# Optimization experiments

Measured on AMD Instinct MI355X. Metric: run time of the kernel, lower is better.

## Reference

```python
import jax, jax.numpy as jnp
import numpy as np

NS = 8          # neighborhood_size
PAD = NS // 2   # pad_size
BW = 0.5        # band_width
EPS_NORM = 1e-12  # F.normalize eps
EPS = 1e-5


def setup_inputs() -> dict:
    key = jax.random.key(0)
    k1, k2, k3, k4, k5 = jax.random.split(key, 5)
    N, C, H, W, D = 2, 48, 64, 64, 64
    S = 10  # num_samples
    x = jax.random.normal(k1, (N, C, H, W, D), dtype=jnp.float32)
    y = jax.random.normal(k2, (N, C, H, W, D), dtype=jnp.float32)
    # torch.randint(pad, H-pad) -> indices in [4, 60)
    h_indices = jax.random.randint(k3, (S,), PAD, H - PAD)
    w_indices = jax.random.randint(k4, (S,), PAD, W - PAD)
    d_indices = jax.random.randint(k5, (S,), PAD, D - PAD)
    return {"x": x, "y": y, "h_indices": h_indices,
            "w_indices": w_indices, "d_indices": d_indices}


def _contextual_loss_3d(x, y, h_idx, w_idx, d_idx):
    N, C = x.shape[0], x.shape[1]

    def slice_neigh(a, hi, wi, di):
        # 8x8x8 cube around (hi, wi, di) -> (N, C, NS, NS, NS)
        return jax.lax.dynamic_slice(
            a, (0, 0, hi - PAD, wi - PAD, di - PAD), (N, C, NS, NS, NS))

    def per_sample(hi, wi, di):
        xn = slice_neigh(x, hi, wi, di).reshape(N, C, -1)  # (N, C, M), M=512
        yn = slice_neigh(y, hi, wi, di).reshape(N, C, -1)
        y_mu = yn.mean(axis=(0, 2), keepdims=True)          # (1, C, 1)
        xc = xn - y_mu
        yc = yn - y_mu
        # F.normalize(p=2, dim=1): divide by max(||.||, eps)
        xc = xc / jnp.maximum(jnp.linalg.norm(xc, axis=1, keepdims=True), EPS_NORM)
        yc = yc / jnp.maximum(jnp.linalg.norm(yc, axis=1, keepdims=True), EPS_NORM)
        dist = 1.0 - jnp.einsum('ncm,ncp->nmp', xc, yc)     # (N, M, M)
        dist_min = dist.min(axis=2, keepdims=True)
        dist_tilde = dist / (dist_min + EPS)
        cx = jax.nn.softmax((1.0 - dist_tilde) / BW, axis=2)
        cx = cx.max(axis=1).mean(axis=1)                    # (N,)
        return jnp.mean(-jnp.log(cx + EPS))

    losses = jax.vmap(per_sample)(h_idx, w_idx, d_idx)      # (S,)
    return losses.mean()


def reference(x, y, h_indices, w_indices, d_indices):
    return _contextual_loss_3d(x, y, h_indices, w_indices, d_indices)
```

## Files before the change

kernel.cpp:

```cpp
#include <hip/hip_runtime.h>
#include <hip/hip_bf16.h>
#include <math.h>

#define S_    10
#define C_    48
#define HWD   64
#define M_    512
#define PADK  4
#define PAIRS 20

#define OFF_GY  0
#define OFF_GX  491520
#define OFF_CM  983040
#define OFF_MU  (OFF_CM + PAIRS * M_)
#define OFF_CNT (OFF_MU + 480)
#define OFF_ALL (OFF_CNT + 20)
#define OFF_PL  (OFF_ALL + 1)
#define OFF_YK  993824
#define OFF_XK  (OFF_YK + 327680)

typedef __attribute__((ext_vector_type(8))) short bf16x8;
typedef __attribute__((ext_vector_type(4))) float f32x4;

__device__ __forceinline__ int gidx(int n, int c, int h, int w, int d) {
  return (((n * C_ + c) * HWD + h) * HWD + w) * HWD + d;
}

__device__ __forceinline__ unsigned short f2bf(float f) {
  unsigned u = __float_as_uint(f);
  u += 0x7FFFu + ((u >> 16) & 1u);
  return (unsigned short)(u >> 16);
}

__device__ __forceinline__ int fidx(int m, int c) {
  return ((m >> 4) << 10) + ((c >> 5) << 9) + (((c >> 3) & 3) << 7) +
         ((m & 15) << 3) + (c & 7);
}

__global__ void k_gather(const float* __restrict__ x, const float* __restrict__ y,
                         const int* __restrict__ hi, const int* __restrict__ wi,
                         const int* __restrict__ di, float* __restrict__ ws) {
  int b = blockIdx.x, t = threadIdx.x;
  int lane = t & 63, wv = t >> 6;
  __shared__ float red[4];
  if (b < 40) ws[OFF_CM + b * 256 + t] = 0.f;
  if (b == 40 && t < 41) ws[OFF_CNT + t] = 0.f;
  int which = b >= 480;
  int r = which ? b - 480 : b;
  int s = r / C_, c = r % C_;
  const float* src = which ? x : y;
  int h0 = hi[s] - PADK, w0 = wi[s] - PADK, d0 = di[s] - PADK;
  float* dst = ws + (which ? OFF_GX : OFF_GY) + (s * 96 + 2 * c) * 512;
  float sum = 0.f;
#pragma unroll
  for (int j = 0; j < 4; ++j) {
    int i = t + 256 * j;
    int n = i >> 9, m = i & 511;
    float v = src[gidx(n, c, h0 + (m >> 6), w0 + ((m >> 3) & 7), d0 + (m & 7))];
    dst[n * 512 + m] = v;
    sum += v;
  }
  if (!which) {
#pragma unroll
    for (int off = 32; off; off >>= 1) sum += __shfl_xor(sum, off);
    if (lane == 0) red[wv] = sum;
    __syncthreads();
    if (t == 0)
      ws[OFF_MU + s * C_ + c] =
          (red[0] + red[1] + red[2] + red[3]) * (1.0f / 1024.0f);
  }
}

__global__ void k_nc(float* __restrict__ ws) {
  int g = blockIdx.x * 256 + threadIdx.x;
  int col = g >> 2;
  int q = threadIdx.x & 3;
  int which = col >= 10240;
  int cix = which ? col - 10240 : col;
  int pair = cix >> 9, m = cix & 511;
  int s = pair >> 1, n = pair & 1;
  const float* base = ws + (which ? OFF_GX : OFF_GY) + (s * 96 + n) * 512 + m;
  const float* mus = ws + OFF_MU + s * C_;
  int c0 = q * 12;
  float v[12], ss = 0.f;
#pragma unroll
  for (int j = 0; j < 12; ++j) {
    v[j] = base[(c0 + j) * 1024] - mus[c0 + j];
    ss += v[j] * v[j];
  }
  ss += __shfl_xor(ss, 1);
  ss += __shfl_xor(ss, 2);
  float sc = 1.0f / fmaxf(sqrtf(ss), 1e-12f);
  unsigned short* dstk = (unsigned short*)(ws + (which ? OFF_XK : OFF_YK)) +
                         pair * 32768;
#pragma unroll
  for (int j = 0; j < 12; ++j) dstk[fidx(m, c0 + j)] = f2bf(v[j] * sc);
  if (q == 3) {
#pragma unroll
    for (int c = 48; c < 64; ++c) dstk[fidx(m, c)] = 0;
  }
}

__global__ __launch_bounds__(64, 2) void k_mm(float* __restrict__ ws,
                                              float* __restrict__ out) {
  int b = blockIdx.x;
  int pair = b >> 5, slab = b & 31;
  int lane = threadIdx.x;

  __shared__ unsigned arr;
  __shared__ int lastflag;

  const unsigned short* xf =
      (const unsigned short*)(ws + OFF_XK) + pair * 32768;
  const unsigned short* yf =
      (const unsigned short*)(ws + OFF_YK) + pair * 32768;

  bf16x8 a0 = *(const bf16x8*)(xf + slab * 1024 + lane * 8);
  bf16x8 a1 = *(const bf16x8*)(xf + slab * 1024 + 512 + lane * 8);

  f32x4 d[32];
#pragma unroll
  for (int ct = 0; ct < 32; ++ct) {
    bf16x8 b0 = *(const bf16x8*)(yf + ct * 1024 + lane * 8);
    bf16x8 b1 = *(const bf16x8*)(yf + ct * 1024 + 512 + lane * 8);
    f32x4 z = {0.f, 0.f, 0.f, 0.f};
    f32x4 dd = __builtin_amdgcn_mfma_f32_16x16x32_bf16(a0, b0, z, 0, 0, 0);
    d[ct] = __builtin_amdgcn_mfma_f32_16x16x32_bf16(a1, b1, dd, 0, 0, 0);
  }

  float am0 = -3.4e38f, am1 = -3.4e38f, am2 = -3.4e38f, am3 = -3.4e38f;
#pragma unroll
  for (int ct = 0; ct < 32; ++ct) {
    am0 = fmaxf(am0, d[ct][0]); am1 = fmaxf(am1, d[ct][1]);
    am2 = fmaxf(am2, d[ct][2]); am3 = fmaxf(am3, d[ct][3]);
  }
#pragma unroll
  for (int off = 1; off < 16; off <<= 1) {
    am0 = fmaxf(am0, __shfl_xor(am0, off));
    am1 = fmaxf(am1, __shfl_xor(am1, off));
    am2 = fmaxf(am2, __shfl_xor(am2, off));
    am3 = fmaxf(am3, __shfl_xor(am3, off));
  }
  float inv0 = 2.f / ((1.f - am0) + 1e-5f), c20 = 2.f - inv0;
  float inv1 = 2.f / ((1.f - am1) + 1e-5f), c21 = 2.f - inv1;
  float inv2 = 2.f / ((1.f - am2) + 1e-5f), c22 = 2.f - inv2;
  float inv3 = 2.f / ((1.f - am3) + 1e-5f), c23 = 2.f - inv3;
  float sm0 = 0.f, sm1 = 0.f, sm2 = 0.f, sm3 = 0.f;
#pragma unroll
  for (int ct = 0; ct < 32; ++ct) {
    float e0 = __expf(fmaf(d[ct][0], inv0, c20));
    float e1 = __expf(fmaf(d[ct][1], inv1, c21));
    float e2 = __expf(fmaf(d[ct][2], inv2, c22));
    float e3 = __expf(fmaf(d[ct][3], inv3, c23));
    d[ct][0] = e0; d[ct][1] = e1; d[ct][2] = e2; d[ct][3] = e3;
    sm0 += e0; sm1 += e1; sm2 += e2; sm3 += e3;
  }
#pragma unroll
  for (int off = 1; off < 16; off <<= 1) {
    sm0 += __shfl_xor(sm0, off); sm1 += __shfl_xor(sm1, off);
    sm2 += __shfl_xor(sm2, off); sm3 += __shfl_xor(sm3, off);
  }
  float rs0 = 1.f / sm0, rs1 = 1.f / sm1, rs2 = 1.f / sm2, rs3 = 1.f / sm3;
  unsigned* cmu = (unsigned*)(ws + OFF_CM) + pair * M_;
#pragma unroll
  for (int ct = 0; ct < 32; ++ct) {
    float cc = fmaxf(fmaxf(d[ct][0] * rs0, d[ct][1] * rs1),
                     fmaxf(d[ct][2] * rs2, d[ct][3] * rs3));
    cc = fmaxf(cc, __shfl_xor(cc, 16));
    cc = fmaxf(cc, __shfl_xor(cc, 32));
    if (lane < 16) atomicMax(&cmu[ct * 16 + lane], __float_as_uint(cc));
  }

  __threadfence();
  if (lane == 0) arr = atomicAdd((unsigned*)(ws + OFF_CNT) + pair, 1u);
  __syncthreads();
  if (arr == 31) {
    float sum = 0.f;
#pragma unroll
    for (int k = 0; k < 8; ++k)
      sum += __uint_as_float(atomicOr(&cmu[lane + 64 * k], 0u));
#pragma unroll
    for (int off = 32; off; off >>= 1) sum += __shfl_xor(sum, off);
    if (lane == 0) {
      lastflag = 0;
      float loss = -logf(sum * (1.0f / 512.0f) + 1e-5f);
      atomicExch((unsigned*)(ws + OFF_PL) + pair, __float_as_uint(loss));
      __threadfence();
      unsigned dct = atomicAdd((unsigned*)(ws + OFF_ALL), 1u);
      if (dct == PAIRS - 1) lastflag = 1;
    }
    __syncthreads();
    if (lastflag && lane < 32) {
      float v = (lane < PAIRS)
                    ? __uint_as_float(atomicOr((unsigned*)(ws + OFF_PL) + lane, 0u))
                    : 0.f;
#pragma unroll
      for (int off = 16; off; off >>= 1) v += __shfl_xor(v, off);
      if (lane == 0) out[0] = v * (1.0f / (float)PAIRS);
    }
  }
}

extern "C" void kernel_launch(void* const* d_in, const int* in_sizes, int n_in,
                              void* d_out, int out_size, void* d_ws, size_t ws_size,
                              hipStream_t stream) {
  const float* x = (const float*)d_in[0];
  const float* y = (const float*)d_in[1];
  const int* hi = (const int*)d_in[2];
  const int* wi = (const int*)d_in[3];
  const int* di = (const int*)d_in[4];
  float* ws = (float*)d_ws;
  float* out = (float*)d_out;

  k_gather<<<960, 256, 0, stream>>>(x, y, hi, wi, di, ws);
  k_nc<<<320, 256, 0, stream>>>(ws);
  k_mm<<<PAIRS * 32, 64, 0, stream>>>(ws, out);
}
```

Before: 38.49 us.

## Split k_mm column tiles across four waves with shared-memory row reductions

The matmul/softmax kernel now uses 256 threads per block, and each of the four waves handles 8 of the 32 column tiles. Per-wave row max and row sums are combined through shared memory with block barriers. This cuts per-thread register pressure and serial work per block, and the cross-wave reduction costs two extra syncs and some LDS traffic.

```diff
diff --git a/kernel.cpp b/kernel.cpp
--- a/kernel.cpp
+++ b/kernel.cpp
@@ -101,12 +101,16 @@
   }
 }
 
-__global__ __launch_bounds__(64, 2) void k_mm(float* __restrict__ ws,
-                                              float* __restrict__ out) {
+__global__ __launch_bounds__(256, 2) void k_mm(float* __restrict__ ws,
+                                               float* __restrict__ out) {
   int b = blockIdx.x;
   int pair = b >> 5, slab = b & 31;
-  int lane = threadIdx.x;
-
+  int t = threadIdx.x, lane = t & 63, wv = t >> 6;
+  int kg = lane >> 4;
+
+  __shared__ float amx[16 * 4];
+  __shared__ float smx[16 * 4];
+  __shared__ float red[4];
   __shared__ unsigned arr;
   __shared__ int lastflag;
 
@@ -118,21 +122,22 @@
   bf16x8 a0 = *(const bf16x8*)(xf + slab * 1024 + lane * 8);
   bf16x8 a1 = *(const bf16x8*)(xf + slab * 1024 + 512 + lane * 8);
 
-  f32x4 d[32];
-#pragma unroll
-  for (int ct = 0; ct < 32; ++ct) {
+  f32x4 d[8];
+#pragma unroll
+  for (int j = 0; j < 8; ++j) {
+    int ct = wv * 8 + j;
     bf16x8 b0 = *(const bf16x8*)(yf + ct * 1024 + lane * 8);
     bf16x8 b1 = *(const bf16x8*)(yf + ct * 1024 + 512 + lane * 8);
     f32x4 z = {0.f, 0.f, 0.f, 0.f};
     f32x4 dd = __builtin_amdgcn_mfma_f32_16x16x32_bf16(a0, b0, z, 0, 0, 0);
-    d[ct] = __builtin_amdgcn_mfma_f32_16x16x32_bf16(a1, b1, dd, 0, 0, 0);
+    d[j] = __builtin_amdgcn_mfma_f32_16x16x32_bf16(a1, b1, dd, 0, 0, 0);
   }
 
   float am0 = -3.4e38f, am1 = -3.4e38f, am2 = -3.4e38f, am3 = -3.4e38f;
 #pragma unroll
-  for (int ct = 0; ct < 32; ++ct) {
-    am0 = fmaxf(am0, d[ct][0]); am1 = fmaxf(am1, d[ct][1]);
-    am2 = fmaxf(am2, d[ct][2]); am3 = fmaxf(am3, d[ct][3]);
+  for (int j = 0; j < 8; ++j) {
+    am0 = fmaxf(am0, d[j][0]); am1 = fmaxf(am1, d[j][1]);
+    am2 = fmaxf(am2, d[j][2]); am3 = fmaxf(am3, d[j][3]);
   }
 #pragma unroll
   for (int off = 1; off < 16; off <<= 1) {
@@ -141,18 +146,36 @@
     am2 = fmaxf(am2, __shfl_xor(am2, off));
     am3 = fmaxf(am3, __shfl_xor(am3, off));
   }
+  if ((lane & 15) == 0) {
+    amx[(kg * 4 + 0) * 4 + wv] = am0;
+    amx[(kg * 4 + 1) * 4 + wv] = am1;
+    amx[(kg * 4 + 2) * 4 + wv] = am2;
+    amx[(kg * 4 + 3) * 4 + wv] = am3;
+  }
+  __syncthreads();
+  {
+    float4 A0 = *(const float4*)&amx[(kg * 4 + 0) * 4];
+    float4 A1 = *(const float4*)&amx[(kg * 4 + 1) * 4];
+    float4 A2 = *(const float4*)&amx[(kg * 4 + 2) * 4];
+    float4 A3 = *(const float4*)&amx[(kg * 4 + 3) * 4];
+    am0 = fmaxf(fmaxf(A0.x, A0.y), fmaxf(A0.z, A0.w));
+    am1 = fmaxf(fmaxf(A1.x, A1.y), fmaxf(A1.z, A1.w));
+    am2 = fmaxf(fmaxf(A2.x, A2.y), fmaxf(A2.z, A2.w));
+    am3 = fmaxf(fmaxf(A3.x, A3.y), fmaxf(A3.z, A3.w));
+  }
   float inv0 = 2.f / ((1.f - am0) + 1e-5f), c20 = 2.f - inv0;
   float inv1 = 2.f / ((1.f - am1) + 1e-5f), c21 = 2.f - inv1;
   float inv2 = 2.f / ((1.f - am2) + 1e-5f), c22 = 2.f - inv2;
   float inv3 = 2.f / ((1.f - am3) + 1e-5f), c23 = 2.f - inv3;
+
   float sm0 = 0.f, sm1 = 0.f, sm2 = 0.f, sm3 = 0.f;
 #pragma unroll
-  for (int ct = 0; ct < 32; ++ct) {
-    float e0 = __expf(fmaf(d[ct][0], inv0, c20));
-    float e1 = __expf(fmaf(d[ct][1], inv1, c21));
-    float e2 = __expf(fmaf(d[ct][2], inv2, c22));
-    float e3 = __expf(fmaf(d[ct][3], inv3, c23));
-    d[ct][0] = e0; d[ct][1] = e1; d[ct][2] = e2; d[ct][3] = e3;
+  for (int j = 0; j < 8; ++j) {
+    float e0 = __expf(fmaf(d[j][0], inv0, c20));
+    float e1 = __expf(fmaf(d[j][1], inv1, c21));
+    float e2 = __expf(fmaf(d[j][2], inv2, c22));
+    float e3 = __expf(fmaf(d[j][3], inv3, c23));
+    d[j][0] = e0; d[j][1] = e1; d[j][2] = e2; d[j][3] = e3;
     sm0 += e0; sm1 += e1; sm2 += e2; sm3 += e3;
   }
 #pragma unroll
@@ -160,43 +183,63 @@
     sm0 += __shfl_xor(sm0, off); sm1 += __shfl_xor(sm1, off);
     sm2 += __shfl_xor(sm2, off); sm3 += __shfl_xor(sm3, off);
   }
-  float rs0 = 1.f / sm0, rs1 = 1.f / sm1, rs2 = 1.f / sm2, rs3 = 1.f / sm3;
+  if ((lane & 15) == 0) {
+    smx[(kg * 4 + 0) * 4 + wv] = sm0;
+    smx[(kg * 4 + 1) * 4 + wv] = sm1;
+    smx[(kg * 4 + 2) * 4 + wv] = sm2;
+    smx[(kg * 4 + 3) * 4 + wv] = sm3;
+  }
+  __syncthreads();
+  float rs0, rs1, rs2, rs3;
+  {
+    float4 S0 = *(const float4*)&smx[(kg * 4 + 0) * 4];
+    float4 S1 = *(const float4*)&smx[(kg * 4 + 1) * 4];
+    float4 S2 = *(const float4*)&smx[(kg * 4 + 2) * 4];
+    float4 S3 = *(const float4*)&smx[(kg * 4 + 3) * 4];
+    rs0 = 1.f / ((S0.x + S0.y) + (S0.z + S0.w));
+    rs1 = 1.f / ((S1.x + S1.y) + (S1.z + S1.w));
+    rs2 = 1.f / ((S2.x + S2.y) + (S2.z + S2.w));
+    rs3 = 1.f / ((S3.x + S3.y) + (S3.z + S3.w));
+  }
+
   unsigned* cmu = (unsigned*)(ws + OFF_CM) + pair * M_;
 #pragma unroll
-  for (int ct = 0; ct < 32; ++ct) {
-    float cc = fmaxf(fmaxf(d[ct][0] * rs0, d[ct][1] * rs1),
-                     fmaxf(d[ct][2] * rs2, d[ct][3] * rs3));
+  for (int j = 0; j < 8; ++j) {
+    int ct = wv * 8 + j;
+    float cc = fmaxf(fmaxf(d[j][0] * rs0, d[j][1] * rs1),
+                     fmaxf(d[j][2] * rs2, d[j][3] * rs3));
     cc = fmaxf(cc, __shfl_xor(cc, 16));
     cc = fmaxf(cc, __shfl_xor(cc, 32));
     if (lane < 16) atomicMax(&cmu[ct * 16 + lane], __float_as_uint(cc));
   }
 
   __threadfence();
-  if (lane == 0) arr = atomicAdd((unsigned*)(ws + OFF_CNT) + pair, 1u);
+  if (t == 0) arr = atomicAdd((unsigned*)(ws + OFF_CNT) + pair, 1u);
   __syncthreads();
   if (arr == 31) {
-    float sum = 0.f;
-#pragma unroll
-    for (int k = 0; k < 8; ++k)
-      sum += __uint_as_float(atomicOr(&cmu[lane + 64 * k], 0u));
+    float sum = __uint_as_float(atomicOr(&cmu[t], 0u)) +
+                __uint_as_float(atomicOr(&cmu[t + 256], 0u));
 #pragma unroll
     for (int off = 32; off; off >>= 1) sum += __shfl_xor(sum, off);
-    if (lane == 0) {
-      lastflag = 0;
-      float loss = -logf(sum * (1.0f / 512.0f) + 1e-5f);
+    if (lane == 0) red[wv] = sum;
+    if (t == 0) lastflag = 0;
+    __syncthreads();
+    if (t == 0) {
+      float tot = red[0] + red[1] + red[2] + red[3];
+      float loss = -logf(tot * (1.0f / 512.0f) + 1e-5f);
       atomicExch((unsigned*)(ws + OFF_PL) + pair, __float_as_uint(loss));
       __threadfence();
       unsigned dct = atomicAdd((unsigned*)(ws + OFF_ALL), 1u);
       if (dct == PAIRS - 1) lastflag = 1;
     }
     __syncthreads();
-    if (lastflag && lane < 32) {
-      float v = (lane < PAIRS)
-                    ? __uint_as_float(atomicOr((unsigned*)(ws + OFF_PL) + lane, 0u))
+    if (lastflag && t < 32) {
+      float v = (t < PAIRS)
+                    ? __uint_as_float(atomicOr((unsigned*)(ws + OFF_PL) + t, 0u))
                     : 0.f;
 #pragma unroll
       for (int off = 16; off; off >>= 1) v += __shfl_xor(v, off);
-      if (lane == 0) out[0] = v * (1.0f / (float)PAIRS);
+      if (t == 0) out[0] = v * (1.0f / (float)PAIRS);
     }
   }
 }
@@ -214,5 +257,5 @@
 
   k_gather<<<960, 256, 0, stream>>>(x, y, hi, wi, di, ws);
   k_nc<<<320, 256, 0, stream>>>(ws);
-  k_mm<<<PAIRS * 32, 64, 0, stream>>>(ws, out);
-}
+  k_mm<<<PAIRS * 32, 256, 0, stream>>>(ws, out);
+}
```

After: 59.03 us. 53.4% more time.

## Replace global atomicMax column reduction with per-slab partials and a final kernel

Applied to the files above, without the earlier changes.

Each k_mm block now writes its per-column max values to a private partial buffer instead of doing atomicMax into a shared per-pair array and running last-block detection. A new k_final kernel reduces the 32 slab partials per pair, computes each pair's loss, and the last pair block averages them. This removes atomic contention, the fence and counter, and the zeroing of the column-max buffer in k_gather. In exchange it adds a fourth kernel launch and extra global traffic for the partial buffer (20x32x512 floats).

```diff
diff --git a/kernel.cpp b/kernel.cpp
--- a/kernel.cpp
+++ b/kernel.cpp
@@ -11,13 +11,14 @@
 
 #define OFF_GY  0
 #define OFF_GX  491520
-#define OFF_CM  983040
-#define OFF_MU  (OFF_CM + PAIRS * M_)
+#define OFF_MU  983040
 #define OFF_CNT (OFF_MU + 480)
 #define OFF_ALL (OFF_CNT + 20)
 #define OFF_PL  (OFF_ALL + 1)
-#define OFF_YK  993824
+#define ZERO_N  (20 + 1 + 20)
+#define OFF_YK  983584
 #define OFF_XK  (OFF_YK + 327680)
+#define OFF_PM  (OFF_XK + 327680)
 
 typedef __attribute__((ext_vector_type(8))) short bf16x8;
 typedef __attribute__((ext_vector_type(4))) float f32x4;
@@ -43,8 +44,7 @@
   int b = blockIdx.x, t = threadIdx.x;
   int lane = t & 63, wv = t >> 6;
   __shared__ float red[4];
-  if (b < 40) ws[OFF_CM + b * 256 + t] = 0.f;
-  if (b == 40 && t < 41) ws[OFF_CNT + t] = 0.f;
+  if (b == 0 && t < ZERO_N) ws[OFF_CNT + t] = 0.f;
   int which = b >= 480;
   int r = which ? b - 480 : b;
   int s = r / C_, c = r % C_;
@@ -101,14 +101,10 @@
   }
 }
 
-__global__ __launch_bounds__(64, 2) void k_mm(float* __restrict__ ws,
-                                              float* __restrict__ out) {
+__global__ __launch_bounds__(64, 2) void k_mm(float* __restrict__ ws) {
   int b = blockIdx.x;
   int pair = b >> 5, slab = b & 31;
   int lane = threadIdx.x;
-
-  __shared__ unsigned arr;
-  __shared__ int lastflag;
 
   const unsigned short* xf =
       (const unsigned short*)(ws + OFF_XK) + pair * 32768;
@@ -161,43 +157,51 @@
     sm2 += __shfl_xor(sm2, off); sm3 += __shfl_xor(sm3, off);
   }
   float rs0 = 1.f / sm0, rs1 = 1.f / sm1, rs2 = 1.f / sm2, rs3 = 1.f / sm3;
-  unsigned* cmu = (unsigned*)(ws + OFF_CM) + pair * M_;
+  float* pm = ws + OFF_PM + (pair * 32 + slab) * M_;
 #pragma unroll
   for (int ct = 0; ct < 32; ++ct) {
     float cc = fmaxf(fmaxf(d[ct][0] * rs0, d[ct][1] * rs1),
                      fmaxf(d[ct][2] * rs2, d[ct][3] * rs3));
     cc = fmaxf(cc, __shfl_xor(cc, 16));
     cc = fmaxf(cc, __shfl_xor(cc, 32));
-    if (lane < 16) atomicMax(&cmu[ct * 16 + lane], __float_as_uint(cc));
-  }
-
-  __threadfence();
-  if (lane == 0) arr = atomicAdd((unsigned*)(ws + OFF_CNT) + pair, 1u);
+    if (lane < 16) pm[ct * 16 + lane] = cc;
+  }
+}
+
+__global__ void k_final(float* __restrict__ ws, float* __restrict__ out) {
+  int pair = blockIdx.x;
+  int t = threadIdx.x, lane = t & 63, wv = t >> 6;
+  __shared__ float red[4];
+  __shared__ int lastflag;
+  const float* pm = ws + OFF_PM + pair * 32 * M_;
+
+  float m0 = 0.f, m1 = 0.f;
+  for (int s = 0; s < 32; ++s) {
+    m0 = fmaxf(m0, pm[s * M_ + t]);
+    m1 = fmaxf(m1, pm[s * M_ + t + 256]);
+  }
+  float sum = m0 + m1;
+#pragma unroll
+  for (int off = 32; off; off >>= 1) sum += __shfl_xor(sum, off);
+  if (lane == 0) red[wv] = sum;
+  if (t == 0) lastflag = 0;
   __syncthreads();
-  if (arr == 31) {
-    float sum = 0.f;
-#pragma unroll
-    for (int k = 0; k < 8; ++k)
-      sum += __uint_as_float(atomicOr(&cmu[lane + 64 * k], 0u));
-#pragma unroll
-    for (int off = 32; off; off >>= 1) sum += __shfl_xor(sum, off);
-    if (lane == 0) {
-      lastflag = 0;
-      float loss = -logf(sum * (1.0f / 512.0f) + 1e-5f);
-      atomicExch((unsigned*)(ws + OFF_PL) + pair, __float_as_uint(loss));
-      __threadfence();
-      unsigned dct = atomicAdd((unsigned*)(ws + OFF_ALL), 1u);
-      if (dct == PAIRS - 1) lastflag = 1;
-    }
-    __syncthreads();
-    if (lastflag && lane < 32) {
-      float v = (lane < PAIRS)
-                    ? __uint_as_float(atomicOr((unsigned*)(ws + OFF_PL) + lane, 0u))
-                    : 0.f;
-#pragma unroll
-      for (int off = 16; off; off >>= 1) v += __shfl_xor(v, off);
-      if (lane == 0) out[0] = v * (1.0f / (float)PAIRS);
-    }
+  if (t == 0) {
+    float tot = red[0] + red[1] + red[2] + red[3];
+    float loss = -logf(tot * (1.0f / 512.0f) + 1e-5f);
+    atomicExch((unsigned*)(ws + OFF_PL) + pair, __float_as_uint(loss));
+    __threadfence();
+    unsigned dct = atomicAdd((unsigned*)(ws + OFF_ALL), 1u);
+    if (dct == PAIRS - 1) lastflag = 1;
+  }
+  __syncthreads();
+  if (lastflag && t < 32) {
+    float v = (t < PAIRS)
+                  ? __uint_as_float(atomicOr((unsigned*)(ws + OFF_PL) + t, 0u))
+                  : 0.f;
+#pragma unroll
+    for (int off = 16; off; off >>= 1) v += __shfl_xor(v, off);
+    if (t == 0) out[0] = v * (1.0f / (float)PAIRS);
   }
 }
 
@@ -214,5 +218,6 @@
 
   k_gather<<<960, 256, 0, stream>>>(x, y, hi, wi, di, ws);
   k_nc<<<320, 256, 0, stream>>>(ws);
-  k_mm<<<PAIRS * 32, 64, 0, stream>>>(ws, out);
-}
+  k_mm<<<PAIRS * 32, 64, 0, stream>>>(ws);
+  k_final<<<PAIRS, 256, 0, stream>>>(ws, out);
+}
```

Measured after the change: 32.13 us, median of 2. 1.2x faster.
